# Kernel tuning notes

Hardware: AMD Instinct MI355X
Metric: run time of the kernel (lower is better)

The kernel has to match this reference:

```python
import jax, jax.numpy as jnp
import numpy as np

DIM = 512
NUM_HEADS = 8
HEAD_DIM = DIM // NUM_HEADS
SCALE = HEAD_DIM ** -0.5


def setup_inputs() -> dict:
    key = jax.random.key(0)
    ks = jax.random.split(key, 11)
    B, T, D = 2, 4096, DIM
    s = 0.02
    return {
        "query": jax.random.normal(ks[0], (B, T, D), jnp.float32),
        "key_": jax.random.normal(ks[1], (B, T, D), jnp.float32),
        "value": jax.random.normal(ks[2], (B, T, D), jnp.float32),
        "Wq": jax.random.normal(ks[3], (D, D), jnp.float32) * s,
        "bq": jnp.zeros((D,), jnp.float32),
        "Wk": jax.random.normal(ks[4], (D, D), jnp.float32) * s,
        "bk": jnp.zeros((D,), jnp.float32),
        "Wv": jax.random.normal(ks[5], (D, D), jnp.float32) * s,
        "bv": jnp.zeros((D,), jnp.float32),
        "Wo": jax.random.normal(ks[6], (D, D), jnp.float32) * s,
        "bo": jnp.zeros((D,), jnp.float32),
    }


def reference(query, key_, value, Wq, bq, Wk, bk, Wv, bv, Wo, bo):
    B, T, D = query.shape
    H, Hd = NUM_HEADS, HEAD_DIM
    # Linear projections (torch Linear: x @ W.T + b)
    q = (query @ Wq.T + bq).reshape(B, T, H, Hd).transpose(0, 2, 1, 3)   # [B,H,T,Hd]
    k = (key_ @ Wk.T + bk).reshape(B, -1, H, Hd).transpose(0, 2, 1, 3)    # [B,H,S,Hd]
    v = (value @ Wv.T + bv).reshape(B, -1, H, Hd).transpose(0, 2, 1, 3)   # [B,H,S,Hd]
    # Full O(T*S) score matrix, as in the original (non-fused) module
    scores = jnp.einsum("bhtd,bhsd->bhts", q, k) * SCALE                  # [B,H,T,S]
    weights = jax.nn.softmax(scores, axis=-1)
    out = jnp.einsum("bhts,bhsd->bhtd", weights, v)                       # [B,H,T,Hd]
    out = out.transpose(0, 2, 1, 3).reshape(B, T, D)
    return out @ Wo.T + bo
```

## Files before the change

### kernel.cpp

```cpp
#include <hip/hip_runtime.h>
#include <cstdint>
#include <cstddef>

typedef __attribute__((ext_vector_type(8)))  __bf16 bf16x8;
typedef __attribute__((ext_vector_type(4)))  float  f32x4;
typedef __attribute__((ext_vector_type(16))) float  f32x16;
typedef __attribute__((ext_vector_type(8)))  unsigned short us8;

#define MFMA(a, b, c)   __builtin_amdgcn_mfma_f32_16x16x32_bf16((a), (b), (c), 0, 0, 0)
#define MFMA32(a, b, c) __builtin_amdgcn_mfma_f32_32x32x16_bf16((a), (b), (c), 0, 0, 0)

#define QSCALE 0.18033688011112042f

__device__ __forceinline__ unsigned short f2bf(float f) {
  unsigned u = __float_as_uint(f);
  u += 0x7fffu + ((u >> 16) & 1u);
  return (unsigned short)(u >> 16);
}

__device__ __forceinline__ float bf2f(unsigned short s) {
  unsigned u = ((unsigned)s) << 16;
  return __uint_as_float(u);
}

__device__ __forceinline__ unsigned pk2bf(float lo, float hi) {
  unsigned a = __float_as_uint(lo) + 0x8000u;
  unsigned b = __float_as_uint(hi) + 0x8000u;
  return __builtin_amdgcn_perm(b, a, 0x07060302u);
}

__device__ __forceinline__ void gload16(const void* g, void* l) {
  __builtin_amdgcn_global_load_lds(
      (__attribute__((address_space(1))) unsigned int*)(uintptr_t)g,
      (__attribute__((address_space(3))) unsigned int*)l,
      16, 0, 0);
}

struct CastArgs {
  const float*    src[7];
  unsigned short* dst[7];
  int             n4[7];
};
__global__ __launch_bounds__(256) void cast_kernel(CastArgs a) {
  int z = blockIdx.y;
  const float* __restrict__ in = a.src[z];
  unsigned short* __restrict__ out = a.dst[z];
  int i = blockIdx.x * 256 + threadIdx.x;
  if (i < a.n4[z]) {
    float4 f = ((const float4*)in)[i];
    ushort4 r;
    r.x = f2bf(f.x); r.y = f2bf(f.y); r.z = f2bf(f.z); r.w = f2bf(f.w);
    ((ushort4*)out)[i] = r;
  }
}

struct ProjArgs {
  const unsigned short* X[3];
  const unsigned short* W[3];
  const float*          bias[3];
  unsigned short*       out[3];
};

__global__ __launch_bounds__(256) void proj_qkv_kernel(ProjArgs args) {
  __shared__ alignas(16) unsigned short smem[16384];

  const int z = blockIdx.z;
  const unsigned short* __restrict__ X   = args.X[z];
  const unsigned short* __restrict__ W   = args.W[z];
  const float* __restrict__ bias         = args.bias[z];
  unsigned short* __restrict__ out       = args.out[z];
  const float scl = (z == 0) ? QSCALE : 1.0f;

  const int t = threadIdx.x;
  const int w = t >> 6, lane = t & 63;
  const int quad = lane >> 4, l15 = lane & 15;
  const int wr = w >> 1, wc = w & 1;
  const int m0 = blockIdx.x * 128, n0 = blockIdx.y * 128;

  const int srow = t >> 2;
  const int scol = (((t & 3) ^ (srow & 3)) << 3);

  f32x4 acc[4][4] = {};

  {
    unsigned short* sA = smem;
    unsigned short* sB = smem + 4096;
    gload16(X + (size_t)(m0 + srow) * 512 + scol,      &sA[w * 512]);
    gload16(X + (size_t)(m0 + srow + 64) * 512 + scol, &sA[2048 + w * 512]);
    gload16(W + (size_t)(n0 + srow) * 512 + scol,      &sB[w * 512]);
    gload16(W + (size_t)(n0 + srow + 64) * 512 + scol, &sB[2048 + w * 512]);
  }

  for (int k0 = 0; k0 < 512; k0 += 32) {
    const int buf = (k0 >> 5) & 1;
    unsigned short* sA = smem + buf * 8192;
    unsigned short* sB = sA + 4096;
    if (k0 < 480) {
      unsigned short* nA = smem + (buf ^ 1) * 8192;
      unsigned short* nB = nA + 4096;
      const int kn = k0 + 32;
      gload16(X + (size_t)(m0 + srow) * 512 + kn + scol,      &nA[w * 512]);
      gload16(X + (size_t)(m0 + srow + 64) * 512 + kn + scol, &nA[2048 + w * 512]);
      gload16(W + (size_t)(n0 + srow) * 512 + kn + scol,      &nB[w * 512]);
      gload16(W + (size_t)(n0 + srow + 64) * 512 + kn + scol, &nB[2048 + w * 512]);
      asm volatile("s_waitcnt vmcnt(4)" ::: "memory");
    } else {
      asm volatile("s_waitcnt vmcnt(0)" ::: "memory");
    }
    __builtin_amdgcn_s_barrier();
    asm volatile("" ::: "memory");

    bf16x8 af[4], bfr[4];
#pragma unroll
    for (int mt = 0; mt < 4; ++mt) {
      int ra = wr * 64 + mt * 16 + l15;
      af[mt] = *(const bf16x8*)&sA[ra * 32 + ((quad ^ (ra & 3)) << 3)];
    }
#pragma unroll
    for (int nt = 0; nt < 4; ++nt) {
      int rb = wc * 64 + nt * 16 + l15;
      bfr[nt] = *(const bf16x8*)&sB[rb * 32 + ((quad ^ (rb & 3)) << 3)];
    }
#pragma unroll
    for (int mt = 0; mt < 4; ++mt)
#pragma unroll
      for (int nt = 0; nt < 4; ++nt)
        acc[mt][nt] = MFMA(af[mt], bfr[nt], acc[mt][nt]);

    asm volatile("" ::: "memory");
    __builtin_amdgcn_s_barrier();
  }

  if (z != 2) {
#pragma unroll
    for (int nt = 0; nt < 4; ++nt) {
      int n = n0 + wc * 64 + nt * 16 + l15;
      float bv = bias[n];
      int h = n >> 6, hd = n & 63;
#pragma unroll
      for (int mt = 0; mt < 4; ++mt) {
#pragma unroll
        for (int r = 0; r < 4; ++r) {
          int m = m0 + wr * 64 + mt * 16 + quad * 4 + r;
          int b = m >> 12, tt = m & 4095;
          out[(((size_t)(b * 8 + h)) * 4096 + tt) * 64 + hd] =
              f2bf((acc[mt][nt][r] + bv) * scl);
        }
      }
    }
  } else {
    const int b   = m0 >> 12;
    const int tt0 = m0 & 4095;
#pragma unroll
    for (int h2 = 0; h2 < 2; ++h2) {
      __syncthreads();
      if (wc == h2) {
#pragma unroll
        for (int nt = 0; nt < 4; ++nt) {
          int nl = nt * 16 + l15;
          float bv = bias[n0 + h2 * 64 + nl];
#pragma unroll
          for (int mt = 0; mt < 4; ++mt)
#pragma unroll
            for (int r = 0; r < 4; ++r) {
              int ml = wr * 64 + mt * 16 + quad * 4 + r;
              smem[nl * 136 + ml] = f2bf((acc[mt][nt][r] + bv) * scl);
            }
        }
      }
      __syncthreads();
      const int row = t >> 2;
      const int c4  = (t & 3) * 8;
      const int n   = n0 + h2 * 64 + row;
      unsigned short* dst = out + ((size_t)(b * 512 + n)) * 4096 + tt0;
#pragma unroll
      for (int k = 0; k < 4; ++k)
        *(us8*)(dst + c4 + k * 32) = *(const us8*)&smem[row * 136 + c4 + k * 32];
    }
  }
}

__global__ __launch_bounds__(256) void proj_out_kernel(
    const unsigned short* __restrict__ X, const unsigned short* __restrict__ W,
    const float* __restrict__ bias, float* __restrict__ out) {
  __shared__ alignas(16) unsigned short smem[16384];

  const int t = threadIdx.x;
  const int w = t >> 6, lane = t & 63;
  const int quad = lane >> 4, l15 = lane & 15;
  const int wr = w >> 1, wc = w & 1;
  const int m0 = blockIdx.x * 128, n0 = blockIdx.y * 128;
  const int srow = t >> 2;
  const int scol = (((t & 3) ^ (srow & 3)) << 3);

  f32x4 acc[4][4] = {};

  {
    unsigned short* sA = smem;
    unsigned short* sB = smem + 4096;
    gload16(X + (size_t)(m0 + srow) * 512 + scol,      &sA[w * 512]);
    gload16(X + (size_t)(m0 + srow + 64) * 512 + scol, &sA[2048 + w * 512]);
    gload16(W + (size_t)(n0 + srow) * 512 + scol,      &sB[w * 512]);
    gload16(W + (size_t)(n0 + srow + 64) * 512 + scol, &sB[2048 + w * 512]);
  }

  for (int k0 = 0; k0 < 512; k0 += 32) {
    const int buf = (k0 >> 5) & 1;
    unsigned short* sA = smem + buf * 8192;
    unsigned short* sB = sA + 4096;
    if (k0 < 480) {
      unsigned short* nA = smem + (buf ^ 1) * 8192;
      unsigned short* nB = nA + 4096;
      const int kn = k0 + 32;
      gload16(X + (size_t)(m0 + srow) * 512 + kn + scol,      &nA[w * 512]);
      gload16(X + (size_t)(m0 + srow + 64) * 512 + kn + scol, &nA[2048 + w * 512]);
      gload16(W + (size_t)(n0 + srow) * 512 + kn + scol,      &nB[w * 512]);
      gload16(W + (size_t)(n0 + srow + 64) * 512 + kn + scol, &nB[2048 + w * 512]);
      asm volatile("s_waitcnt vmcnt(4)" ::: "memory");
    } else {
      asm volatile("s_waitcnt vmcnt(0)" ::: "memory");
    }
    __builtin_amdgcn_s_barrier();
    asm volatile("" ::: "memory");

    bf16x8 af[4], bfr[4];
#pragma unroll
    for (int mt = 0; mt < 4; ++mt) {
      int ra = wr * 64 + mt * 16 + l15;
      af[mt] = *(const bf16x8*)&sA[ra * 32 + ((quad ^ (ra & 3)) << 3)];
    }
#pragma unroll
    for (int nt = 0; nt < 4; ++nt) {
      int rb = wc * 64 + nt * 16 + l15;
      bfr[nt] = *(const bf16x8*)&sB[rb * 32 + ((quad ^ (rb & 3)) << 3)];
    }
#pragma unroll
    for (int mt = 0; mt < 4; ++mt)
#pragma unroll
      for (int nt = 0; nt < 4; ++nt)
        acc[mt][nt] = MFMA(af[mt], bfr[nt], acc[mt][nt]);

    asm volatile("" ::: "memory");
    __builtin_amdgcn_s_barrier();
  }

#pragma unroll
  for (int nt = 0; nt < 4; ++nt) {
    int n = n0 + wc * 64 + nt * 16 + l15;
    float bv = bias[n];
#pragma unroll
    for (int mt = 0; mt < 4; ++mt) {
#pragma unroll
      for (int r = 0; r < 4; ++r) {
        int m = m0 + wr * 64 + mt * 16 + quad * 4 + r;
        out[(size_t)m * 512 + n] = acc[mt][nt][r] + bv;
      }
    }
  }
}

__global__ __launch_bounds__(256, 4) void attn_kernel(
    const unsigned short* __restrict__ Q, const unsigned short* __restrict__ K,
    const unsigned short* __restrict__ VT,
    unsigned short* __restrict__ pO0, unsigned short* __restrict__ pO1,
    float* __restrict__ pL) {
  __shared__ alignas(16) unsigned short kt[2][4096];
  __shared__ alignas(16) unsigned short vt[2][4096];

  const int t = threadIdx.x;
  const int w = t >> 6, lane = t & 63;
  const int l31 = lane & 31, h = lane >> 5;

  const int wg  = blockIdx.x + gridDim.x * blockIdx.y;
  const int swz = (wg & 7) * 128 + (wg >> 3);
  const int bx  = swz & 31;
  const int bh2 = swz >> 5;
  const int bh  = bh2 & 15, half = bh2 >> 4;

  const unsigned short* __restrict__ Qp  = Q  + (size_t)bh * 4096 * 64;
  const unsigned short* __restrict__ Kp  = K  + (size_t)bh * 4096 * 64;
  const unsigned short* __restrict__ VTp = VT + (size_t)bh * 64 * 4096;

  const int q0w = bx * 128 + w * 32;
  const int sbase = half * 2048;

  const int grow = t >> 3;
  const int gcol = (((t & 7) ^ (grow & 7)) << 3);

#define STAGE(bbuf, s0)                                                        \
  {                                                                            \
    gload16(Kp + (size_t)((s0) + grow) * 64 + gcol,        &kt[bbuf][w * 512]);\
    gload16(Kp + (size_t)((s0) + grow + 32) * 64 + gcol,                       \
            &kt[bbuf][2048 + w * 512]);                                        \
    gload16(VTp + (size_t)grow * 4096 + (s0) + gcol,       &vt[bbuf][w * 512]);\
    gload16(VTp + (size_t)(grow + 32) * 4096 + (s0) + gcol,                    \
            &vt[bbuf][2048 + w * 512]);                                        \
  }

  STAGE(0, sbase);

  bf16x8 aq[4];
#pragma unroll
  for (int kd = 0; kd < 4; ++kd)
    aq[kd] = *(const bf16x8*)(Qp + (size_t)(q0w + l31) * 64 + kd * 16 + h * 8);

  union { unsigned short s[8]; bf16x8 v; } one_u;
#pragma unroll
  for (int i = 0; i < 8; ++i) one_u.s[i] = 0x3F80;
  const bf16x8 ones = one_u.v;

  f32x16 o0 = {}, o1 = {}, lsum = {};

  const int swzk = (l31 & 7);

  for (int j = 0; j < 32; ++j) {
    const int cb = j & 1, nb = cb ^ 1;
    if (j < 31) {
      STAGE(nb, sbase + (j + 1) * 64);
      asm volatile("s_waitcnt vmcnt(4)" ::: "memory");
    } else {
      asm volatile("s_waitcnt vmcnt(0)" ::: "memory");
    }
    __builtin_amdgcn_s_barrier();
    asm volatile("" ::: "memory");

    const unsigned short* ktb = kt[cb];
    const unsigned short* vtb = vt[cb];

#pragma unroll
    for (int st = 0; st < 2; ++st) {
      f32x16 scv = {};
#pragma unroll
      for (int kd = 0; kd < 4; ++kd) {
        bf16x8 kf = *(const bf16x8*)&ktb[(st * 32 + l31) * 64 +
                                         (((2 * kd + h) ^ swzk) << 3)];
        scv = MFMA32(kf, aq[kd], scv);
      }

      float p[16];
#pragma unroll
      for (int r = 0; r < 16; ++r) p[r] = __builtin_amdgcn_exp2f(scv[r]);
      unsigned Xg[4], Yg[4];
#pragma unroll
      for (int g = 0; g < 4; ++g) {
        Xg[g] = pk2bf(p[4 * g + 0], p[4 * g + 1]);
        Yg[g] = pk2bf(p[4 * g + 2], p[4 * g + 3]);
      }

#pragma unroll
      for (int ks = 0; ks < 2; ++ks) {
        unsigned Lx = h ? Xg[2 * ks + 1] : Xg[2 * ks];
        unsigned Mx = h ? Xg[2 * ks]     : Xg[2 * ks + 1];
        unsigned Ly = h ? Yg[2 * ks + 1] : Yg[2 * ks];
        unsigned My = h ? Yg[2 * ks]     : Yg[2 * ks + 1];
        unsigned sMx = (unsigned)__shfl_xor((int)Mx, 32, 64);
        unsigned sMy = (unsigned)__shfl_xor((int)My, 32, 64);
        union { unsigned u[4]; bf16x8 v; } pa;
        pa.u[0] = h ? sMx : Lx;
        pa.u[1] = h ? sMy : Ly;
        pa.u[2] = h ? Lx  : sMx;
        pa.u[3] = h ? Ly  : sMy;
        const int c = st * 4 + 2 * ks + h;
        bf16x8 v0 = *(const bf16x8*)&vtb[l31 * 64 + ((c ^ swzk) << 3)];
        bf16x8 v1 = *(const bf16x8*)&vtb[(l31 + 32) * 64 +
                                         ((c ^ ((l31 + 32) & 7)) << 3)];
        o0 = MFMA32(pa.v, v0, o0);
        o1 = MFMA32(pa.v, v1, o1);
        lsum = MFMA32(pa.v, ones, lsum);
      }
    }

    asm volatile("" ::: "memory");
    __builtin_amdgcn_s_barrier();
  }
#undef STAGE

  unsigned short* __restrict__ PO = half ? pO1 : pO0;
  float* __restrict__ PLh = pL + half * 65536 + bh * 4096;
  const int bq = bh >> 3, hh = bh & 7;
#pragma unroll
  for (int r = 0; r < 16; ++r) {
    const int qloc = (r & 3) + 8 * (r >> 2) + 4 * h;
    const int trow = q0w + qloc;
    const size_t base = ((size_t)bq * 4096 + trow) * 512 + hh * 64;
    PO[base + l31]      = f2bf(o0[r]);
    PO[base + 32 + l31] = f2bf(o1[r]);
    if (l31 == 0) PLh[trow] = lsum[r];
  }
}

__global__ __launch_bounds__(256) void combine_kernel(
    const unsigned short* __restrict__ p0, const unsigned short* __restrict__ p1,
    const float* __restrict__ pL, unsigned short* __restrict__ ao) {
  const int i = blockIdx.x * 256 + threadIdx.x;
  const int idx8 = i * 8;
  const int col = idx8 & 511;
  const int t   = (idx8 >> 9) & 4095;
  const int bq  = idx8 >> 21;
  const int bh  = bq * 8 + (col >> 6);
  const float inv = 1.0f / (pL[bh * 4096 + t] + pL[65536 + bh * 4096 + t]);
  us8 a = *(const us8*)&p0[idx8];
  us8 b = *(const us8*)&p1[idx8];
  us8 o;
#pragma unroll
  for (int k = 0; k < 8; ++k)
    o[k] = f2bf((bf2f(a[k]) + bf2f(b[k])) * inv);
  *(us8*)&ao[idx8] = o;
}

extern "C" void kernel_launch(void* const* d_in, const int* in_sizes, int n_in,
                              void* d_out, int out_size, void* d_ws, size_t ws_size,
                              hipStream_t stream) {
  (void)in_sizes; (void)n_in; (void)out_size; (void)ws_size;
  const float* query = (const float*)d_in[0];
  const float* key_  = (const float*)d_in[1];
  const float* value = (const float*)d_in[2];
  const float* Wq = (const float*)d_in[3];
  const float* bq = (const float*)d_in[4];
  const float* Wk = (const float*)d_in[5];
  const float* bk = (const float*)d_in[6];
  const float* Wv = (const float*)d_in[7];
  const float* bv = (const float*)d_in[8];
  const float* Wo = (const float*)d_in[9];
  const float* bo = (const float*)d_in[10];
  float* out = (float*)d_out;

  char* ws = (char*)d_ws;
  const size_t MB = 1024 * 1024;
  unsigned short* Xq  = (unsigned short*)(ws + 0 * MB);
  unsigned short* Xk  = (unsigned short*)(ws + 8 * MB);
  unsigned short* Xv  = (unsigned short*)(ws + 16 * MB);
  unsigned short* Wqb = (unsigned short*)(ws + 24 * MB);
  unsigned short* Wkb = (unsigned short*)(ws + 24 * MB + 512 * 1024);
  unsigned short* Wvb = (unsigned short*)(ws + 25 * MB);
  unsigned short* qb  = (unsigned short*)(ws + 26 * MB);
  unsigned short* kb  = (unsigned short*)(ws + 34 * MB);
  unsigned short* vtb = (unsigned short*)(ws + 42 * MB);
  unsigned short* Wob = (unsigned short*)(ws + 58 * MB);
  unsigned short* pO0 = (unsigned short*)(ws + 0 * MB);
  unsigned short* pO1 = (unsigned short*)(ws + 9 * MB);
  float*          pL  = (float*)(ws + 18 * MB);
  unsigned short* ao  = (unsigned short*)(ws + 42 * MB);

  CastArgs ca;
  ca.src[0] = query; ca.src[1] = key_; ca.src[2] = value;
  ca.src[3] = Wq;    ca.src[4] = Wk;   ca.src[5] = Wv;  ca.src[6] = Wo;
  ca.dst[0] = Xq;    ca.dst[1] = Xk;   ca.dst[2] = Xv;
  ca.dst[3] = Wqb;   ca.dst[4] = Wkb;  ca.dst[5] = Wvb; ca.dst[6] = Wob;
  ca.n4[0] = ca.n4[1] = ca.n4[2] = 1048576;
  ca.n4[3] = ca.n4[4] = ca.n4[5] = ca.n4[6] = 65536;
  cast_kernel<<<dim3(4096, 7), 256, 0, stream>>>(ca);

  ProjArgs pa;
  pa.X[0] = Xq;  pa.X[1] = Xk;  pa.X[2] = Xv;
  pa.W[0] = Wqb; pa.W[1] = Wkb; pa.W[2] = Wvb;
  pa.bias[0] = bq; pa.bias[1] = bk; pa.bias[2] = bv;
  pa.out[0] = qb; pa.out[1] = kb; pa.out[2] = vtb;
  proj_qkv_kernel<<<dim3(64, 4, 3), 256, 0, stream>>>(pa);

  attn_kernel<<<dim3(32, 32), 256, 0, stream>>>(qb, kb, vtb, pO0, pO1, pL);

  combine_kernel<<<dim3(2048), 256, 0, stream>>>(pO0, pO1, pL, ao);

  proj_out_kernel<<<dim3(64, 4), 256, 0, stream>>>(ao, Wob, bo, out);
}
```

Measured before the change: 240.4 us.

## Give each attention wave two 32-row Q tiles and drop the ones-MFMA row sum

The attention kernel now runs 2 waves per block, each handling 64 query rows split into two 32-row tiles. Each K fragment and V fragment read from LDS is reused across both tiles, halving LDS reads per MFMA. The row-sum MFMA against a ones vector is replaced by a scalar add tree plus one cross-half shuffle at the end. The shuffle-and-select packing of P is replaced by v_permlane32_swap. The trade-offs are higher register pressure, fewer waves per block to hide latency, and per-wave staging loads that double to 8 in flight.

```diff
diff --git a/kernel.cpp b/kernel.cpp
--- a/kernel.cpp
+++ b/kernel.cpp
@@ -27,6 +27,10 @@
   unsigned a = __float_as_uint(lo) + 0x8000u;
   unsigned b = __float_as_uint(hi) + 0x8000u;
   return __builtin_amdgcn_perm(b, a, 0x07060302u);
+}
+
+__device__ __forceinline__ void pl32swap(unsigned& a, unsigned& b) {
+  asm("v_permlane32_swap_b32 %0, %1" : "+v"(a), "+v"(b));
 }
 
 __device__ __forceinline__ void gload16(const void* g, void* l) {
@@ -34,6 +38,14 @@
       (__attribute__((address_space(1))) unsigned int*)(uintptr_t)g,
       (__attribute__((address_space(3))) unsigned int*)l,
       16, 0, 0);
+}
+
+__device__ __forceinline__ float tree16(const float* p) {
+  float a = (p[0] + p[1]) + (p[2] + p[3]);
+  float b = (p[4] + p[5]) + (p[6] + p[7]);
+  float c = (p[8] + p[9]) + (p[10] + p[11]);
+  float d = (p[12] + p[13]) + (p[14] + p[15]);
+  return (a + b) + (c + d);
 }
 
 struct CastArgs {
@@ -259,7 +271,7 @@
   }
 }
 
-__global__ __launch_bounds__(256, 4) void attn_kernel(
+__global__ __launch_bounds__(128, 2) void attn_kernel(
     const unsigned short* __restrict__ Q, const unsigned short* __restrict__ K,
     const unsigned short* __restrict__ VT,
     unsigned short* __restrict__ pO0, unsigned short* __restrict__ pO1,
@@ -268,12 +280,13 @@
   __shared__ alignas(16) unsigned short vt[2][4096];
 
   const int t = threadIdx.x;
-  const int w = t >> 6, lane = t & 63;
+  const int w = t >> 6;
+  const int lane = t & 63;
   const int l31 = lane & 31, h = lane >> 5;
 
   const int wg  = blockIdx.x + gridDim.x * blockIdx.y;
   const int swz = (wg & 7) * 128 + (wg >> 3);
-  const int bx  = swz & 31;
+  const int qt  = swz & 31;
   const int bh2 = swz >> 5;
   const int bh  = bh2 & 15, half = bh2 >> 4;
 
@@ -281,43 +294,43 @@
   const unsigned short* __restrict__ Kp  = K  + (size_t)bh * 4096 * 64;
   const unsigned short* __restrict__ VTp = VT + (size_t)bh * 64 * 4096;
 
-  const int q0w = bx * 128 + w * 32;
+  const int q0w = qt * 128 + w * 64;
   const int sbase = half * 2048;
 
-  const int grow = t >> 3;
-  const int gcol = (((t & 7) ^ (grow & 7)) << 3);
+  const int lr   = lane >> 3;
+  const int gcol = (((lane & 7) ^ lr) << 3);
 
 #define STAGE(bbuf, s0)                                                        \
   {                                                                            \
-    gload16(Kp + (size_t)((s0) + grow) * 64 + gcol,        &kt[bbuf][w * 512]);\
-    gload16(Kp + (size_t)((s0) + grow + 32) * 64 + gcol,                       \
-            &kt[bbuf][2048 + w * 512]);                                        \
-    gload16(VTp + (size_t)grow * 4096 + (s0) + gcol,       &vt[bbuf][w * 512]);\
-    gload16(VTp + (size_t)(grow + 32) * 4096 + (s0) + gcol,                    \
-            &vt[bbuf][2048 + w * 512]);                                        \
+    _Pragma("unroll")                                                          \
+    for (int i = 0; i < 4; ++i)                                                \
+      gload16(Kp + (size_t)((s0) + w * 32 + i * 8 + lr) * 64 + gcol,           \
+              &kt[bbuf][(w * 32 + i * 8) * 64]);                               \
+    _Pragma("unroll")                                                          \
+    for (int i = 0; i < 4; ++i)                                                \
+      gload16(VTp + (size_t)(w * 32 + i * 8 + lr) * 4096 + (s0) + gcol,        \
+              &vt[bbuf][(w * 32 + i * 8) * 64]);                               \
   }
 
   STAGE(0, sbase);
 
-  bf16x8 aq[4];
-#pragma unroll
-  for (int kd = 0; kd < 4; ++kd)
-    aq[kd] = *(const bf16x8*)(Qp + (size_t)(q0w + l31) * 64 + kd * 16 + h * 8);
-
-  union { unsigned short s[8]; bf16x8 v; } one_u;
-#pragma unroll
-  for (int i = 0; i < 8; ++i) one_u.s[i] = 0x3F80;
-  const bf16x8 ones = one_u.v;
-
-  f32x16 o0 = {}, o1 = {}, lsum = {};
-
-  const int swzk = (l31 & 7);
+  bf16x8 aqA[4], aqB[4];
+#pragma unroll
+  for (int kd = 0; kd < 4; ++kd) {
+    aqA[kd] = *(const bf16x8*)(Qp + (size_t)(q0w + l31) * 64 + kd * 16 + h * 8);
+    aqB[kd] = *(const bf16x8*)(Qp + (size_t)(q0w + 32 + l31) * 64 + kd * 16 + h * 8);
+  }
+
+  f32x16 o0a = {}, o1a = {}, o0b = {}, o1b = {};
+  float lia = 0.f, lib = 0.f;
+
+  const int swzk = l31 & 7;
 
   for (int j = 0; j < 32; ++j) {
     const int cb = j & 1, nb = cb ^ 1;
     if (j < 31) {
       STAGE(nb, sbase + (j + 1) * 64);
-      asm volatile("s_waitcnt vmcnt(4)" ::: "memory");
+      asm volatile("s_waitcnt vmcnt(8)" ::: "memory");
     } else {
       asm volatile("s_waitcnt vmcnt(0)" ::: "memory");
     }
@@ -329,44 +342,59 @@
 
 #pragma unroll
     for (int st = 0; st < 2; ++st) {
-      f32x16 scv = {};
+      bf16x8 kf[4];
+#pragma unroll
+      for (int kd = 0; kd < 4; ++kd)
+        kf[kd] = *(const bf16x8*)&ktb[(st * 32 + l31) * 64 +
+                                      (((2 * kd + h) ^ swzk) << 3)];
+      f32x16 sa = {}, sb = {};
 #pragma unroll
       for (int kd = 0; kd < 4; ++kd) {
-        bf16x8 kf = *(const bf16x8*)&ktb[(st * 32 + l31) * 64 +
-                                         (((2 * kd + h) ^ swzk) << 3)];
-        scv = MFMA32(kf, aq[kd], scv);
-      }
-
-      float p[16];
-#pragma unroll
-      for (int r = 0; r < 16; ++r) p[r] = __builtin_amdgcn_exp2f(scv[r]);
-      unsigned Xg[4], Yg[4];
+        sa = MFMA32(kf[kd], aqA[kd], sa);
+        sb = MFMA32(kf[kd], aqB[kd], sb);
+      }
+
+      float pA[16], pB[16];
+#pragma unroll
+      for (int r = 0; r < 16; ++r) {
+        pA[r] = __builtin_amdgcn_exp2f(sa[r]);
+        pB[r] = __builtin_amdgcn_exp2f(sb[r]);
+      }
+      lia += tree16(pA);
+      lib += tree16(pB);
+
+      unsigned XgA[4], YgA[4], XgB[4], YgB[4];
 #pragma unroll
       for (int g = 0; g < 4; ++g) {
-        Xg[g] = pk2bf(p[4 * g + 0], p[4 * g + 1]);
-        Yg[g] = pk2bf(p[4 * g + 2], p[4 * g + 3]);
+        XgA[g] = pk2bf(pA[4 * g + 0], pA[4 * g + 1]);
+        YgA[g] = pk2bf(pA[4 * g + 2], pA[4 * g + 3]);
+        XgB[g] = pk2bf(pB[4 * g + 0], pB[4 * g + 1]);
+        YgB[g] = pk2bf(pB[4 * g + 2], pB[4 * g + 3]);
       }
 
 #pragma unroll
       for (int ks = 0; ks < 2; ++ks) {
-        unsigned Lx = h ? Xg[2 * ks + 1] : Xg[2 * ks];
-        unsigned Mx = h ? Xg[2 * ks]     : Xg[2 * ks + 1];
-        unsigned Ly = h ? Yg[2 * ks + 1] : Yg[2 * ks];
-        unsigned My = h ? Yg[2 * ks]     : Yg[2 * ks + 1];
-        unsigned sMx = (unsigned)__shfl_xor((int)Mx, 32, 64);
-        unsigned sMy = (unsigned)__shfl_xor((int)My, 32, 64);
-        union { unsigned u[4]; bf16x8 v; } pa;
-        pa.u[0] = h ? sMx : Lx;
-        pa.u[1] = h ? sMy : Ly;
-        pa.u[2] = h ? Lx  : sMx;
-        pa.u[3] = h ? Ly  : sMy;
         const int c = st * 4 + 2 * ks + h;
         bf16x8 v0 = *(const bf16x8*)&vtb[l31 * 64 + ((c ^ swzk) << 3)];
-        bf16x8 v1 = *(const bf16x8*)&vtb[(l31 + 32) * 64 +
-                                         ((c ^ ((l31 + 32) & 7)) << 3)];
-        o0 = MFMA32(pa.v, v0, o0);
-        o1 = MFMA32(pa.v, v1, o1);
-        lsum = MFMA32(pa.v, ones, lsum);
+        bf16x8 v1 = *(const bf16x8*)&vtb[(l31 + 32) * 64 + ((c ^ swzk) << 3)];
+
+        unsigned a0 = XgA[2 * ks], a2 = XgA[2 * ks + 1];
+        unsigned a1 = YgA[2 * ks], a3 = YgA[2 * ks + 1];
+        pl32swap(a0, a2);
+        pl32swap(a1, a3);
+        union { unsigned u[4]; bf16x8 v; } paA;
+        paA.u[0] = a0; paA.u[1] = a1; paA.u[2] = a2; paA.u[3] = a3;
+        o0a = MFMA32(paA.v, v0, o0a);
+        o1a = MFMA32(paA.v, v1, o1a);
+
+        unsigned b0 = XgB[2 * ks], b2 = XgB[2 * ks + 1];
+        unsigned b1 = YgB[2 * ks], b3 = YgB[2 * ks + 1];
+        pl32swap(b0, b2);
+        pl32swap(b1, b3);
+        union { unsigned u[4]; bf16x8 v; } paB;
+        paB.u[0] = b0; paB.u[1] = b1; paB.u[2] = b2; paB.u[3] = b3;
+        o0b = MFMA32(paB.v, v0, o0b);
+        o1b = MFMA32(paB.v, v1, o1b);
       }
     }
 
@@ -375,17 +403,25 @@
   }
 #undef STAGE
 
+  lia += __shfl_xor(lia, 32, 64);
+  lib += __shfl_xor(lib, 32, 64);
+  float* __restrict__ PLh = pL + half * 65536 + bh * 4096;
+  if (h == 0) {
+    PLh[q0w + l31]      = lia;
+    PLh[q0w + 32 + l31] = lib;
+  }
+
   unsigned short* __restrict__ PO = half ? pO1 : pO0;
-  float* __restrict__ PLh = pL + half * 65536 + bh * 4096;
   const int bq = bh >> 3, hh = bh & 7;
 #pragma unroll
   for (int r = 0; r < 16; ++r) {
     const int qloc = (r & 3) + 8 * (r >> 2) + 4 * h;
-    const int trow = q0w + qloc;
-    const size_t base = ((size_t)bq * 4096 + trow) * 512 + hh * 64;
-    PO[base + l31]      = f2bf(o0[r]);
-    PO[base + 32 + l31] = f2bf(o1[r]);
-    if (l31 == 0) PLh[trow] = lsum[r];
+    const size_t baseA = ((size_t)bq * 4096 + q0w + qloc) * 512 + hh * 64;
+    PO[baseA + l31]      = f2bf(o0a[r]);
+    PO[baseA + 32 + l31] = f2bf(o1a[r]);
+    const size_t baseB = ((size_t)bq * 4096 + q0w + 32 + qloc) * 512 + hh * 64;
+    PO[baseB + l31]      = f2bf(o0b[r]);
+    PO[baseB + 32 + l31] = f2bf(o1b[r]);
   }
 }
 
@@ -458,7 +494,7 @@
   pa.out[0] = qb; pa.out[1] = kb; pa.out[2] = vtb;
   proj_qkv_kernel<<<dim3(64, 4, 3), 256, 0, stream>>>(pa);
 
-  attn_kernel<<<dim3(32, 32), 256, 0, stream>>>(qb, kb, vtb, pO0, pO1, pL);
+  attn_kernel<<<dim3(32, 32), 128, 0, stream>>>(qb, kb, vtb, pO0, pO1, pL);
 
   combine_kernel<<<dim3(2048), 256, 0, stream>>>(pO0, pO1, pL, ao);
 
```

Result: no change. 236.1 us (-1.8%).
